# Kernel tuning notes

Measured on AMD Instinct MI355X. Metric: run time of the kernel, lower is better.

## Reference

```python
import jax, jax.numpy as jnp
import numpy as np

B, T, D = 2, 2048, 1024
N, K, H = 16, 8, 128  # q heads, kv heads, head_dim
G = N // K            # GQA group size
EPS = 1e-6
THETA = 1000000.0
SCALE = H ** -0.5
K_MASK = float(np.finfo(np.float32).min)


def rms_norm(x, scale):
    # RMSNorm over head_dim (last axis), computed in fp32 like the original
    dtype = x.dtype
    rms = jnp.sqrt(jnp.mean(x.astype(jnp.float32) ** 2, axis=-1, keepdims=True) + EPS)
    return (scale * x / rms).astype(dtype)


def positions_from_segment_ids(seg):
    t = jnp.arange(seg.shape[1], dtype=jnp.int32)[None, :]
    off = jnp.argmax(seg, axis=1, keepdims=True).astype(jnp.int32)
    rel = t - off
    return jnp.where(seg != 0, rel, jnp.int32(2 ** 30))


def rope_sin_cos(positions):
    frac = jnp.arange(0, H, 2, dtype=jnp.float32) / H
    inv_freq = 1.0 / (THETA ** frac)                    # [H/2]
    ang = positions.astype(jnp.float32)[..., None] * inv_freq  # [B,T,H/2]
    return jnp.sin(ang), jnp.cos(ang)


def apply_rope(x, sin, cos):
    # x: [B,T,heads,H]; sin/cos: [B,T,H/2]
    x1, x2 = x[..., : H // 2], x[..., H // 2:]
    s, c = sin[:, :, None, :], cos[:, :, None, :]
    return jnp.concatenate([x1 * c - x2 * s, x2 * c + x1 * s], axis=-1).astype(x.dtype)


def setup_inputs() -> dict:
    key = jax.random.key(0)
    ks = jax.random.split(key, 8)
    std = 0.02
    return {
        "x": jax.random.normal(ks[0], (B, T, D), dtype=jnp.float32),
        "segment_ids": jnp.ones((B, T), dtype=jnp.int32),
        "wq": jax.random.normal(ks[1], (D, N, H), dtype=jnp.float32) * std,
        "wk": jax.random.normal(ks[2], (D, K, H), dtype=jnp.float32) * std,
        "wv": jax.random.normal(ks[3], (D, K, H), dtype=jnp.float32) * std,
        "wo": jax.random.normal(ks[4], (N, H, D), dtype=jnp.float32) * std,
        "q_scale": jnp.ones((H,), dtype=jnp.float32),
        "k_scale": jnp.ones((H,), dtype=jnp.float32),
    }


def reference(x, segment_ids, wq, wk, wv, wo, q_scale, k_scale):
    # QKV projections + QK RMSNorm
    q = rms_norm(jnp.einsum('BTD,DNH->BTNH', x, wq), q_scale)  # [B,T,N,H]
    k = rms_norm(jnp.einsum('BSD,DKH->BSKH', x, wk), k_scale)  # [B,T,K,H]
    v = jnp.einsum('BSD,DKH->BSKH', x, wv)                     # [B,T,K,H]

    # RoPE using segment-relative positions
    pos = positions_from_segment_ids(segment_ids)  # [B,T] int32
    sin, cos = rope_sin_cos(pos)
    q = apply_rope(q, sin, cos)
    k = apply_rope(k, sin, cos)

    # GQA attention: [B,T,K,G,H] x [B,S,K,H] -> [B,T,S,K,G]
    qg = q.reshape(B, T, K, G, H)
    logits = jnp.einsum('BTKGH,BSKH->BTSKG', qg, k) * SCALE

    causal = pos[:, None, :] <= pos[:, :, None]                       # [B,T,S]
    segm = segment_ids[:, None, :] == segment_ids[:, :, None]         # [B,T,S]
    mask = (causal & segm)[:, :, :, None, None]
    logits = jnp.where(mask, logits, K_MASK)

    w = jax.nn.softmax(logits.astype(jnp.float32), axis=2).astype(logits.dtype)
    out = jnp.einsum('BTSKG,BSKH->BTKGH', w, v).reshape(B, T, N, H)
    return jnp.einsum('BTNH,NHD->BTD', out, wo)
```

## Files before the change

kernel.cpp:

```cpp
#include <hip/hip_runtime.h>
#include <hip/hip_bf16.h>


typedef unsigned short u16;
typedef __attribute__((ext_vector_type(8))) short s16x8;
typedef __attribute__((ext_vector_type(4))) float fp32x4;
typedef __attribute__((ext_vector_type(4))) u16 u16x4;

#define MFMA_BF16(a, b, c) __builtin_amdgcn_mfma_f32_16x16x32_bf16((a), (b), (c), 0, 0, 0)

static constexpr int Bq = 2, Tq = 2048, Dq = 1024, NHq = 16, KHq = 8, Hq = 128;
static constexpr float EPSq = 1e-6f;
static constexpr float S2q = 0.08838834764831845f * 1.4426950408889634f;
static constexpr float MAXq = 20.0f;
static constexpr float NEGHUGE = -3.0e38f;

__device__ __forceinline__ u16 f2b(float f) {
  __hip_bfloat16 h = __float2bfloat16(f);
  return *reinterpret_cast<u16*>(&h);
}

__device__ __forceinline__ void gload16(const u16* g, u16* lds_base) {
  __builtin_amdgcn_global_load_lds(
      (const __attribute__((address_space(1))) unsigned int*)(const void*)g,
      (__attribute__((address_space(3))) unsigned int*)(void*)lds_base, 16, 0, 0);
}


__global__ __launch_bounds__(256) void prep_kernel(
    const float* __restrict__ x, const float* __restrict__ wq,
    const float* __restrict__ wk, const float* __restrict__ wv,
    const float* __restrict__ wo, const int* __restrict__ seg,
    u16* __restrict__ xb, u16* __restrict__ wqkv_t, u16* __restrict__ wo_t,
    int* __restrict__ pos) {
  const int bid = blockIdx.x;
  const int tid = threadIdx.x;
  if (bid < 4096) {
    const int i = bid * 1024 + tid * 4;
    const float4 v = *reinterpret_cast<const float4*>(x + i);
    u16x4 o;
    o.x = f2b(v.x); o.y = f2b(v.y); o.z = f2b(v.z); o.w = f2b(v.w);
    *reinterpret_cast<u16x4*>(xb + i) = o;
    return;
  }
  __shared__ float tile[32][33];
  __shared__ int sv[256], si[256];
  const int tx = tid & 31, ty = tid >> 5;
  if (bid < 8192) {
    const int z = bid - 4096;
    const int r0 = (z & 31) * 32;
    const int c0 = (z >> 5) * 32;
    const float* src;
    int stride, coff;
    if (c0 < 2048)      { src = wq; stride = 2048; coff = c0; }
    else if (c0 < 3072) { src = wk; stride = 1024; coff = c0 - 2048; }
    else                { src = wv; stride = 1024; coff = c0 - 3072; }
#pragma unroll
    for (int j = 0; j < 32; j += 8)
      tile[ty + j][tx] = src[(long)(r0 + ty + j) * stride + (coff + tx)];
    __syncthreads();
#pragma unroll
    for (int j = 0; j < 32; j += 8)
      wqkv_t[(long)(c0 + ty + j) * 1024 + (r0 + tx)] = f2b(tile[tx][ty + j]);
    return;
  }
  if (bid < 10240) {
    const int z = bid - 8192;
    const int c0 = (z & 31) * 32;
    const int r0 = (z >> 5) * 32;
#pragma unroll
    for (int j = 0; j < 32; j += 8)
      tile[ty + j][tx] = wo[(long)(r0 + ty + j) * 1024 + (c0 + tx)];
    __syncthreads();
#pragma unroll
    for (int j = 0; j < 32; j += 8)
      wo_t[(long)(c0 + ty + j) * 2048 + (r0 + tx)] = f2b(tile[tx][ty + j]);
    return;
  }
  const int b = bid - 10240;
  const int* s = seg + b * Tq;
  int bestv = -2147483647 - 1, besti = 0x7fffffff;
  for (int t = tid; t < Tq; t += 256) {
    int v = s[t];
    if (v > bestv) { bestv = v; besti = t; }
  }
  sv[tid] = bestv; si[tid] = besti;
  __syncthreads();
  for (int k = 128; k > 0; k >>= 1) {
    if (tid < k) {
      int v2 = sv[tid + k], i2 = si[tid + k];
      if (v2 > sv[tid] || (v2 == sv[tid] && i2 < si[tid])) {
        sv[tid] = v2; si[tid] = i2;
      }
    }
    __syncthreads();
  }
  const int off = si[0];
  for (int t = tid; t < Tq; t += 256)
    pos[b * Tq + t] = (s[t] != 0) ? (t - off) : (1 << 30);
}


__global__ __launch_bounds__(256) void gemm_qkv_kernel(
    const u16* __restrict__ A, const u16* __restrict__ Bt,
    u16* __restrict__ qkv, u16* __restrict__ vt, const int* __restrict__ pos,
    const float* __restrict__ q_scale, const float* __restrict__ k_scale) {
  __shared__ __align__(16) u16 As[128][64];
  __shared__ __align__(16) u16 Bs[128][64];
  const int tid = threadIdx.x;
  const int wave = tid >> 6, lane = tid & 63;
  const int quad = lane >> 4, l16 = lane & 15;
  const int m0 = blockIdx.y * 128, n0 = blockIdx.x * 128;
  const int row8 = lane >> 3;
  const int cgl = (lane & 7) ^ row8;

  const fp32x4 z4 = {0.f, 0.f, 0.f, 0.f};
  fp32x4 acc[2][8];
#pragma unroll
  for (int i = 0; i < 2; ++i)
#pragma unroll
    for (int j = 0; j < 8; ++j) acc[i][j] = z4;

  for (int k0 = 0; k0 < 1024; k0 += 64) {
    __syncthreads();
#pragma unroll
    for (int jj = 0; jj < 4; ++jj) {
      const int R = wave * 32 + jj * 8;
      gload16(A + (size_t)(m0 + R + row8) * 1024 + k0 + cgl * 8, &As[R][0]);
      gload16(Bt + (size_t)(n0 + R + row8) * 1024 + k0 + cgl * 8, &Bs[R][0]);
    }
    __syncthreads();
#pragma unroll
    for (int kh = 0; kh < 2; ++kh) {
      s16x8 af[2], bfr[8];
#pragma unroll
      for (int i = 0; i < 2; ++i)
        af[i] = *(const s16x8*)&As[wave * 32 + i * 16 + l16]
                               [((((kh << 2) | quad) ^ (l16 & 7)) << 3)];
#pragma unroll
      for (int j = 0; j < 8; ++j)
        bfr[j] = *(const s16x8*)&Bs[j * 16 + l16]
                                [((((kh << 2) | quad) ^ (l16 & 7)) << 3)];
#pragma unroll
      for (int i = 0; i < 2; ++i)
#pragma unroll
        for (int j = 0; j < 8; ++j) acc[i][j] = MFMA_BF16(af[i], bfr[j], acc[i][j]);
    }
  }

  const int wrow = m0 + wave * 32;
  if (n0 >= 3072) {
    const int kv8 = (n0 - 3072) >> 7;
    const int bq = wrow >> 11;
    const size_t vbase = (size_t)(bq * KHq + kv8) * Hq * Tq;
#pragma unroll
    for (int i = 0; i < 2; ++i) {
      const int t = (wrow + i * 16 + quad * 4) & 2047;
#pragma unroll
      for (int j = 0; j < 8; ++j) {
        const int h = j * 16 + l16;
        u16x4 o;
#pragma unroll
        for (int r = 0; r < 4; ++r) o[r] = f2b(acc[i][j][r]);
        *reinterpret_cast<u16x4*>(&vt[vbase + (size_t)h * Tq + t]) = o;
      }
    }
    return;
  }
  const float* scp = (n0 < 2048) ? q_scale : k_scale;
  float scl[8];
#pragma unroll
  for (int j = 0; j < 8; ++j) scl[j] = scp[j * 16 + l16];
  float invf[4];
#pragma unroll
  for (int jf = 0; jf < 4; ++jf)
    invf[jf] = __builtin_amdgcn_exp2f(
                   -(float)(jf * 16 + l16) * (19.931568569324174f / 64.0f)) *
               0.15915494309189535f;
#pragma unroll
  for (int i = 0; i < 2; ++i) {
    float ss[4] = {0.f, 0.f, 0.f, 0.f};
#pragma unroll
    for (int j = 0; j < 8; ++j)
#pragma unroll
      for (int r = 0; r < 4; ++r) ss[r] += acc[i][j][r] * acc[i][j][r];
#pragma unroll
    for (int d = 1; d < 16; d <<= 1)
#pragma unroll
      for (int r = 0; r < 4; ++r) ss[r] += __shfl_xor(ss[r], d, 64);
#pragma unroll
    for (int r = 0; r < 4; ++r) {
      const int row = wrow + i * 16 + quad * 4 + r;
      const float rinv = rsqrtf(ss[r] * (1.0f / 128.0f) + EPSq);
      const float P = (float)pos[row];
      u16* orow = qkv + (size_t)row * 4096 + n0;
#pragma unroll
      for (int jf = 0; jf < 4; ++jf) {
        float rev = P * invf[jf];
        rev -= floorf(rev);
        const float s = __builtin_amdgcn_sinf(rev);
        const float c = __builtin_amdgcn_cosf(rev);
        const float a1 = acc[i][jf][r] * rinv * scl[jf];
        const float a2 = acc[i][jf + 4][r] * rinv * scl[jf + 4];
        orow[jf * 16 + l16] = f2b(a1 * c - a2 * s);
        orow[(jf + 4) * 16 + l16] = f2b(a2 * c + a1 * s);
      }
    }
  }
}


__global__ __launch_bounds__(256) void gemm_out_kernel(
    const u16* __restrict__ A, const u16* __restrict__ Bt,
    float* __restrict__ C) {
  __shared__ __align__(16) u16 As[128][64];
  __shared__ __align__(16) u16 Bs[64][64];
  const int tid = threadIdx.x;
  const int wave = tid >> 6, lane = tid & 63;
  const int quad = lane >> 4, l16 = lane & 15;
  const int m0 = blockIdx.y * 128, n0 = blockIdx.x * 64;
  const int wm = (wave >> 1) * 64, wn = (wave & 1) * 32;
  const int row8 = lane >> 3;
  const int cgl = (lane & 7) ^ row8;

  const fp32x4 z4 = {0.f, 0.f, 0.f, 0.f};
  fp32x4 acc[4][2];
#pragma unroll
  for (int i = 0; i < 4; ++i)
#pragma unroll
    for (int j = 0; j < 2; ++j) acc[i][j] = z4;

  for (int k0 = 0; k0 < 2048; k0 += 64) {
    __syncthreads();
#pragma unroll
    for (int jj = 0; jj < 4; ++jj) {
      const int R = wave * 32 + jj * 8;
      gload16(A + (size_t)(m0 + R + row8) * 2048 + k0 + cgl * 8, &As[R][0]);
    }
#pragma unroll
    for (int jj = 0; jj < 2; ++jj) {
      const int R = wave * 16 + jj * 8;
      gload16(Bt + (size_t)(n0 + R + row8) * 2048 + k0 + cgl * 8, &Bs[R][0]);
    }
    __syncthreads();
#pragma unroll
    for (int kh = 0; kh < 2; ++kh) {
      s16x8 af[4], bfr[2];
#pragma unroll
      for (int i = 0; i < 4; ++i)
        af[i] = *(const s16x8*)&As[wm + i * 16 + l16]
                               [((((kh << 2) | quad) ^ (l16 & 7)) << 3)];
#pragma unroll
      for (int j = 0; j < 2; ++j)
        bfr[j] = *(const s16x8*)&Bs[wn + j * 16 + l16]
                                [((((kh << 2) | quad) ^ (l16 & 7)) << 3)];
#pragma unroll
      for (int i = 0; i < 4; ++i)
#pragma unroll
        for (int j = 0; j < 2; ++j) acc[i][j] = MFMA_BF16(af[i], bfr[j], acc[i][j]);
    }
  }
#pragma unroll
  for (int i = 0; i < 4; ++i) {
    const int row = m0 + wm + i * 16 + quad * 4;
#pragma unroll
    for (int j = 0; j < 2; ++j) {
      const int col = n0 + wn + j * 16 + l16;
#pragma unroll
      for (int r = 0; r < 4; ++r)
        C[(size_t)(row + r) * 1024 + col] = acc[i][j][r];
    }
  }
}


__global__ __launch_bounds__(256, 1) void flash_kernel(
    const u16* __restrict__ qkv, const u16* __restrict__ vt,
    const int* __restrict__ pos, const int* __restrict__ seg,
    u16* __restrict__ Obuf) {
  const int tid = threadIdx.x;
  const int w = tid >> 6;
  const int lane = tid & 63;
  const int quad = lane >> 4, l16 = lane & 15;
  const int g = blockIdx.x;
  const int b = g & 1;
  const int kv = (g >> 1) & 7;
  const int qh = kv * 2 + ((g >> 4) & 1);
  const int p = g >> 5;

  __shared__ __align__(16) u16 Ks[2][64][128];
  __shared__ __align__(16) u16 Vs[2][128][64];
  __shared__ __align__(16) u16 Ps[4][32][72];

  const u16* kbase = qkv + (size_t)(b * Tq) * 4096 + 2048 + kv * Hq;
  const u16* vbase = vt + (size_t)(b * KHq + kv) * Hq * Tq;
  const int krow_off = lane >> 4;
  const int vrow_off = lane >> 3;
  const fp32x4 z4 = {0.f, 0.f, 0.f, 0.f};
  const short one_bf = (short)0x3F80;
  const s16x8 ones = {one_bf, one_bf, one_bf, one_bf,
                      one_bf, one_bf, one_bf, one_bf};

  auto STAGE = [&](int bi, int st) {
    const int s0 = st * 64;
#pragma unroll
    for (int j = 0; j < 4; ++j) {
      const int R = w * 16 + j * 4;
      const int r = R + krow_off;
      const int cg = (lane & 15) ^ (r & 15);
      gload16(kbase + (size_t)(s0 + r) * 4096 + cg * 8, &Ks[bi][R][0]);
    }
#pragma unroll
    for (int j = 0; j < 4; ++j) {
      const int R = w * 32 + j * 8;
      const int r = R + vrow_off;
      const int cg = (lane & 7) ^ (vrow_off & 7);
      gload16(vbase + (size_t)r * Tq + s0 + cg * 8, &Vs[bi][R][0]);
    }
  };

#pragma unroll
  for (int phase = 0; phase < 2; ++phase) {
    const int c = phase ? p : 15 - p;
    const int t0 = c * 128 + w * 32;
    const int nst = 2 * (c + 1);

    s16x8 qf[2][4];
    int my_pos[2][4], my_seg[2][4];
#pragma unroll
    for (int rb = 0; rb < 2; ++rb) {
      const u16* qrow =
          qkv + (size_t)(b * Tq + t0 + rb * 16 + l16) * 4096 + qh * Hq;
#pragma unroll
      for (int ks = 0; ks < 4; ++ks)
        qf[rb][ks] = *(const s16x8*)(qrow + ks * 32 + quad * 8);
#pragma unroll
      for (int i = 0; i < 4; ++i) {
        const int t = t0 + rb * 16 + quad * 4 + i;
        my_pos[rb][i] = pos[b * Tq + t];
        my_seg[rb][i] = seg[b * Tq + t];
      }
    }
    fp32x4 l_acc[2] = {z4, z4};
    fp32x4 o_acc[2][8];
#pragma unroll
    for (int rb = 0; rb < 2; ++rb)
#pragma unroll
      for (int h = 0; h < 8; ++h) o_acc[rb][h] = z4;

    STAGE(0, 0);
    __syncthreads();

    for (int st = 0; st < nst; ++st) {
      const int cur = st & 1;
      if (st + 1 < nst) STAGE(cur ^ 1, st + 1);

      fp32x4 sc[2][4];
#pragma unroll
      for (int rb = 0; rb < 2; ++rb)
#pragma unroll
        for (int sub = 0; sub < 4; ++sub) sc[rb][sub] = z4;
#pragma unroll
      for (int sub = 0; sub < 4; ++sub)
#pragma unroll
        for (int ks = 0; ks < 4; ++ks) {
          const s16x8 kf = *(const s16x8*)&Ks[cur][sub * 16 + l16]
                                             [((((ks << 2) | quad) ^ l16) << 3)];
          sc[0][sub] = MFMA_BF16(qf[0][ks], kf, sc[0][sub]);
          sc[1][sub] = MFMA_BF16(qf[1][ks], kf, sc[1][sub]);
        }

      const int s0 = st * 64;
      if (st >= nst - 2) {
        int spos[4], sseg[4];
#pragma unroll
        for (int sub = 0; sub < 4; ++sub) {
          const int s = s0 + sub * 16 + l16;
          spos[sub] = pos[b * Tq + s];
          sseg[sub] = seg[b * Tq + s];
        }
#pragma unroll
        for (int rb = 0; rb < 2; ++rb)
#pragma unroll
          for (int sub = 0; sub < 4; ++sub)
#pragma unroll
            for (int i = 0; i < 4; ++i) {
              const bool ok = (sseg[sub] == my_seg[rb][i]) &&
                              (spos[sub] <= my_pos[rb][i]);
              sc[rb][sub][i] = ok ? sc[rb][sub][i] * S2q - MAXq : NEGHUGE;
            }
      } else {
#pragma unroll
        for (int rb = 0; rb < 2; ++rb)
#pragma unroll
          for (int sub = 0; sub < 4; ++sub)
#pragma unroll
            for (int i = 0; i < 4; ++i)
              sc[rb][sub][i] = sc[rb][sub][i] * S2q - MAXq;
      }

#pragma unroll
      for (int rb = 0; rb < 2; ++rb)
#pragma unroll
        for (int sub = 0; sub < 4; ++sub)
#pragma unroll
          for (int i = 0; i < 4; ++i)
            Ps[w][rb * 16 + quad * 4 + i][sub * 16 + l16] =
                f2b(__builtin_amdgcn_exp2f(sc[rb][sub][i]));
      asm volatile("s_waitcnt lgkmcnt(0)" ::: "memory");
      s16x8 pf[2][2];
#pragma unroll
      for (int rb = 0; rb < 2; ++rb)
#pragma unroll
        for (int kk = 0; kk < 2; ++kk)
          pf[rb][kk] = *(const s16x8*)&Ps[w][rb * 16 + l16][kk * 32 + quad * 8];

      l_acc[0] = MFMA_BF16(pf[0][0], ones, l_acc[0]);
      l_acc[0] = MFMA_BF16(pf[0][1], ones, l_acc[0]);
      l_acc[1] = MFMA_BF16(pf[1][0], ones, l_acc[1]);
      l_acc[1] = MFMA_BF16(pf[1][1], ones, l_acc[1]);
#pragma unroll
      for (int j = 0; j < 8; ++j)
#pragma unroll
        for (int kk = 0; kk < 2; ++kk) {
          const s16x8 vf =
              *(const s16x8*)&Vs[cur][j * 16 + l16]
                             [((((kk << 2) | quad) ^ (l16 & 7)) << 3)];
          o_acc[0][j] = MFMA_BF16(pf[0][kk], vf, o_acc[0][j]);
          o_acc[1][j] = MFMA_BF16(pf[1][kk], vf, o_acc[1][j]);
        }

      __syncthreads();
    }

#pragma unroll
    for (int rb = 0; rb < 2; ++rb) {
      float inv[4];
#pragma unroll
      for (int i = 0; i < 4; ++i)
        inv[i] = (l_acc[rb][i] > 0.f) ? 1.f / l_acc[rb][i] : 0.f;
#pragma unroll
      for (int j = 0; j < 8; ++j)
#pragma unroll
        for (int i = 0; i < 4; ++i) {
          const int t = t0 + rb * 16 + quad * 4 + i;
          Obuf[(size_t)(b * Tq + t) * 2048 + qh * Hq + j * 16 + l16] =
              f2b(o_acc[rb][j][i] * inv[i]);
        }
    }
  }
}


extern "C" void kernel_launch(void* const* d_in, const int* in_sizes, int n_in,
                              void* d_out, int out_size, void* d_ws, size_t ws_size,
                              hipStream_t stream) {
  const float* x = (const float*)d_in[0];
  const int* seg = (const int*)d_in[1];
  const float* wq = (const float*)d_in[2];
  const float* wk = (const float*)d_in[3];
  const float* wv = (const float*)d_in[4];
  const float* wo = (const float*)d_in[5];
  const float* q_scale = (const float*)d_in[6];
  const float* k_scale = (const float*)d_in[7];
  float* out = (float*)d_out;

  char* ws = (char*)d_ws;
  u16* xb = (u16*)(ws);
  u16* wqkv_t = (u16*)(ws + 8388608);
  u16* qkv = (u16*)(ws + 16777216);
  u16* vt = (u16*)(ws + 50331648);
  u16* wo_t = (u16*)(ws + 58720256);
  u16* Obuf = (u16*)(ws + 62914560);
  int* posb = (int*)(ws + 79691776);

  prep_kernel<<<10242, 256, 0, stream>>>(x, wq, wk, wv, wo, seg,
                                         xb, wqkv_t, wo_t, posb);

  gemm_qkv_kernel<<<dim3(32, 32, 1), 256, 0, stream>>>(
      xb, wqkv_t, qkv, vt, posb, q_scale, k_scale);

  flash_kernel<<<256, 256, 0, stream>>>(qkv, vt, posb, seg, Obuf);

  gemm_out_kernel<<<dim3(16, 32, 1), 256, 0, stream>>>(Obuf, wo_t, out);
}
```

Before: 235.0 us.

## Split flash kernel causal phases into separate blocks and drop LDS double buffering

Each flash block previously handled two query chunks (c and 15-p) sequentially with double-buffered K/V LDS staging. Now the grid doubles to 512 blocks, each handling one chunk, K/V staging becomes single-buffered with syncs around each load, and launch bounds allow two blocks per CU. The aim is more resident waves and latency hiding through occupancy instead of in-block prefetch. The cost is that loads are no longer overlapped with compute inside a block, and per-block work is now unbalanced across the causal chunks.

After: 237.9 us. Within noise of the previous version (+1.2%).

```diff
diff --git a/kernel.cpp b/kernel.cpp
--- a/kernel.cpp
+++ b/kernel.cpp
@@ -274,7 +274,7 @@
 }
 
 
-__global__ __launch_bounds__(256, 1) void flash_kernel(
+__global__ __launch_bounds__(256, 2) void flash_kernel(
     const u16* __restrict__ qkv, const u16* __restrict__ vt,
     const int* __restrict__ pos, const int* __restrict__ seg,
     u16* __restrict__ Obuf) {
@@ -283,13 +283,17 @@
   const int lane = tid & 63;
   const int quad = lane >> 4, l16 = lane & 15;
   const int g = blockIdx.x;
-  const int b = g & 1;
-  const int kv = (g >> 1) & 7;
-  const int qh = kv * 2 + ((g >> 4) & 1);
-  const int p = g >> 5;
-
-  __shared__ __align__(16) u16 Ks[2][64][128];
-  __shared__ __align__(16) u16 Vs[2][128][64];
+  const int u = g & 255;
+  const int b = u & 1;
+  const int kv = (u >> 1) & 7;
+  const int qh = kv * 2 + ((u >> 4) & 1);
+  const int p = u >> 5;
+  const int c = (g >> 8) ? p : 15 - p;
+  const int t0 = c * 128 + w * 32;
+  const int nst = 2 * (c + 1);
+
+  __shared__ __align__(16) u16 Ks[64][128];
+  __shared__ __align__(16) u16 Vs[128][64];
   __shared__ __align__(16) u16 Ps[4][32][72];
 
   const u16* kbase = qkv + (size_t)(b * Tq) * 4096 + 2048 + kv * Hq;
@@ -301,153 +305,137 @@
   const s16x8 ones = {one_bf, one_bf, one_bf, one_bf,
                       one_bf, one_bf, one_bf, one_bf};
 
-  auto STAGE = [&](int bi, int st) {
+  s16x8 qf[2][4];
+  int my_pos[2][4], my_seg[2][4];
+#pragma unroll
+  for (int rb = 0; rb < 2; ++rb) {
+    const u16* qrow =
+        qkv + (size_t)(b * Tq + t0 + rb * 16 + l16) * 4096 + qh * Hq;
+#pragma unroll
+    for (int ks = 0; ks < 4; ++ks)
+      qf[rb][ks] = *(const s16x8*)(qrow + ks * 32 + quad * 8);
+#pragma unroll
+    for (int i = 0; i < 4; ++i) {
+      const int t = t0 + rb * 16 + quad * 4 + i;
+      my_pos[rb][i] = pos[b * Tq + t];
+      my_seg[rb][i] = seg[b * Tq + t];
+    }
+  }
+  fp32x4 l_acc[2] = {z4, z4};
+  fp32x4 o_acc[2][8];
+#pragma unroll
+  for (int rb = 0; rb < 2; ++rb)
+#pragma unroll
+    for (int h = 0; h < 8; ++h) o_acc[rb][h] = z4;
+
+  for (int st = 0; st < nst; ++st) {
     const int s0 = st * 64;
+    __syncthreads();
 #pragma unroll
     for (int j = 0; j < 4; ++j) {
       const int R = w * 16 + j * 4;
       const int r = R + krow_off;
       const int cg = (lane & 15) ^ (r & 15);
-      gload16(kbase + (size_t)(s0 + r) * 4096 + cg * 8, &Ks[bi][R][0]);
+      gload16(kbase + (size_t)(s0 + r) * 4096 + cg * 8, &Ks[R][0]);
     }
 #pragma unroll
     for (int j = 0; j < 4; ++j) {
       const int R = w * 32 + j * 8;
       const int r = R + vrow_off;
       const int cg = (lane & 7) ^ (vrow_off & 7);
-      gload16(vbase + (size_t)r * Tq + s0 + cg * 8, &Vs[bi][R][0]);
-    }
-  };
-
-#pragma unroll
-  for (int phase = 0; phase < 2; ++phase) {
-    const int c = phase ? p : 15 - p;
-    const int t0 = c * 128 + w * 32;
-    const int nst = 2 * (c + 1);
-
-    s16x8 qf[2][4];
-    int my_pos[2][4], my_seg[2][4];
-#pragma unroll
-    for (int rb = 0; rb < 2; ++rb) {
-      const u16* qrow =
-          qkv + (size_t)(b * Tq + t0 + rb * 16 + l16) * 4096 + qh * Hq;
-#pragma unroll
-      for (int ks = 0; ks < 4; ++ks)
-        qf[rb][ks] = *(const s16x8*)(qrow + ks * 32 + quad * 8);
+      gload16(vbase + (size_t)r * Tq + s0 + cg * 8, &Vs[R][0]);
+    }
+    __syncthreads();
+
+    fp32x4 sc[2][4];
+#pragma unroll
+    for (int rb = 0; rb < 2; ++rb)
+#pragma unroll
+      for (int sub = 0; sub < 4; ++sub) sc[rb][sub] = z4;
+#pragma unroll
+    for (int sub = 0; sub < 4; ++sub)
+#pragma unroll
+      for (int ks = 0; ks < 4; ++ks) {
+        const s16x8 kf = *(const s16x8*)&Ks[sub * 16 + l16]
+                                           [((((ks << 2) | quad) ^ l16) << 3)];
+        sc[0][sub] = MFMA_BF16(qf[0][ks], kf, sc[0][sub]);
+        sc[1][sub] = MFMA_BF16(qf[1][ks], kf, sc[1][sub]);
+      }
+
+    if (st >= nst - 2) {
+      int spos[4], sseg[4];
+#pragma unroll
+      for (int sub = 0; sub < 4; ++sub) {
+        const int s = s0 + sub * 16 + l16;
+        spos[sub] = pos[b * Tq + s];
+        sseg[sub] = seg[b * Tq + s];
+      }
+#pragma unroll
+      for (int rb = 0; rb < 2; ++rb)
+#pragma unroll
+        for (int sub = 0; sub < 4; ++sub)
+#pragma unroll
+          for (int i = 0; i < 4; ++i) {
+            const bool ok = (sseg[sub] == my_seg[rb][i]) &&
+                            (spos[sub] <= my_pos[rb][i]);
+            sc[rb][sub][i] = ok ? sc[rb][sub][i] * S2q - MAXq : NEGHUGE;
+          }
+    } else {
+#pragma unroll
+      for (int rb = 0; rb < 2; ++rb)
+#pragma unroll
+        for (int sub = 0; sub < 4; ++sub)
+#pragma unroll
+          for (int i = 0; i < 4; ++i)
+            sc[rb][sub][i] = sc[rb][sub][i] * S2q - MAXq;
+    }
+
+#pragma unroll
+    for (int rb = 0; rb < 2; ++rb)
+#pragma unroll
+      for (int sub = 0; sub < 4; ++sub)
+#pragma unroll
+        for (int i = 0; i < 4; ++i)
+          Ps[w][rb * 16 + quad * 4 + i][sub * 16 + l16] =
+              f2b(__builtin_amdgcn_exp2f(sc[rb][sub][i]));
+    asm volatile("s_waitcnt lgkmcnt(0)" ::: "memory");
+    s16x8 pf[2][2];
+#pragma unroll
+    for (int rb = 0; rb < 2; ++rb)
+#pragma unroll
+      for (int kk = 0; kk < 2; ++kk)
+        pf[rb][kk] = *(const s16x8*)&Ps[w][rb * 16 + l16][kk * 32 + quad * 8];
+
+    l_acc[0] = MFMA_BF16(pf[0][0], ones, l_acc[0]);
+    l_acc[0] = MFMA_BF16(pf[0][1], ones, l_acc[0]);
+    l_acc[1] = MFMA_BF16(pf[1][0], ones, l_acc[1]);
+    l_acc[1] = MFMA_BF16(pf[1][1], ones, l_acc[1]);
+#pragma unroll
+    for (int j = 0; j < 8; ++j)
+#pragma unroll
+      for (int kk = 0; kk < 2; ++kk) {
+        const s16x8 vf =
+            *(const s16x8*)&Vs[j * 16 + l16]
+                           [((((kk << 2) | quad) ^ (l16 & 7)) << 3)];
+        o_acc[0][j] = MFMA_BF16(pf[0][kk], vf, o_acc[0][j]);
+        o_acc[1][j] = MFMA_BF16(pf[1][kk], vf, o_acc[1][j]);
+      }
+  }
+
+#pragma unroll
+  for (int rb = 0; rb < 2; ++rb) {
+    float inv[4];
+#pragma unroll
+    for (int i = 0; i < 4; ++i)
+      inv[i] = (l_acc[rb][i] > 0.f) ? 1.f / l_acc[rb][i] : 0.f;
+#pragma unroll
+    for (int j = 0; j < 8; ++j)
 #pragma unroll
       for (int i = 0; i < 4; ++i) {
         const int t = t0 + rb * 16 + quad * 4 + i;
-        my_pos[rb][i] = pos[b * Tq + t];
-        my_seg[rb][i] = seg[b * Tq + t];
-      }
-    }
-    fp32x4 l_acc[2] = {z4, z4};
-    fp32x4 o_acc[2][8];
-#pragma unroll
-    for (int rb = 0; rb < 2; ++rb)
-#pragma unroll
-      for (int h = 0; h < 8; ++h) o_acc[rb][h] = z4;
-
-    STAGE(0, 0);
-    __syncthreads();
-
-    for (int st = 0; st < nst; ++st) {
-      const int cur = st & 1;
-      if (st + 1 < nst) STAGE(cur ^ 1, st + 1);
-
-      fp32x4 sc[2][4];
-#pragma unroll
-      for (int rb = 0; rb < 2; ++rb)
-#pragma unroll
-        for (int sub = 0; sub < 4; ++sub) sc[rb][sub] = z4;
-#pragma unroll
-      for (int sub = 0; sub < 4; ++sub)
-#pragma unroll
-        for (int ks = 0; ks < 4; ++ks) {
-          const s16x8 kf = *(const s16x8*)&Ks[cur][sub * 16 + l16]
-                                             [((((ks << 2) | quad) ^ l16) << 3)];
-          sc[0][sub] = MFMA_BF16(qf[0][ks], kf, sc[0][sub]);
-          sc[1][sub] = MFMA_BF16(qf[1][ks], kf, sc[1][sub]);
-        }
-
-      const int s0 = st * 64;
-      if (st >= nst - 2) {
-        int spos[4], sseg[4];
-#pragma unroll
-        for (int sub = 0; sub < 4; ++sub) {
-          const int s = s0 + sub * 16 + l16;
-          spos[sub] = pos[b * Tq + s];
-          sseg[sub] = seg[b * Tq + s];
-        }
-#pragma unroll
-        for (int rb = 0; rb < 2; ++rb)
-#pragma unroll
-          for (int sub = 0; sub < 4; ++sub)
-#pragma unroll
-            for (int i = 0; i < 4; ++i) {
-              const bool ok = (sseg[sub] == my_seg[rb][i]) &&
-                              (spos[sub] <= my_pos[rb][i]);
-              sc[rb][sub][i] = ok ? sc[rb][sub][i] * S2q - MAXq : NEGHUGE;
-            }
-      } else {
-#pragma unroll
-        for (int rb = 0; rb < 2; ++rb)
-#pragma unroll
-          for (int sub = 0; sub < 4; ++sub)
-#pragma unroll
-            for (int i = 0; i < 4; ++i)
-              sc[rb][sub][i] = sc[rb][sub][i] * S2q - MAXq;
-      }
-
-#pragma unroll
-      for (int rb = 0; rb < 2; ++rb)
-#pragma unroll
-        for (int sub = 0; sub < 4; ++sub)
-#pragma unroll
-          for (int i = 0; i < 4; ++i)
-            Ps[w][rb * 16 + quad * 4 + i][sub * 16 + l16] =
-                f2b(__builtin_amdgcn_exp2f(sc[rb][sub][i]));
-      asm volatile("s_waitcnt lgkmcnt(0)" ::: "memory");
-      s16x8 pf[2][2];
-#pragma unroll
-      for (int rb = 0; rb < 2; ++rb)
-#pragma unroll
-        for (int kk = 0; kk < 2; ++kk)
-          pf[rb][kk] = *(const s16x8*)&Ps[w][rb * 16 + l16][kk * 32 + quad * 8];
-
-      l_acc[0] = MFMA_BF16(pf[0][0], ones, l_acc[0]);
-      l_acc[0] = MFMA_BF16(pf[0][1], ones, l_acc[0]);
-      l_acc[1] = MFMA_BF16(pf[1][0], ones, l_acc[1]);
-      l_acc[1] = MFMA_BF16(pf[1][1], ones, l_acc[1]);
-#pragma unroll
-      for (int j = 0; j < 8; ++j)
-#pragma unroll
-        for (int kk = 0; kk < 2; ++kk) {
-          const s16x8 vf =
-              *(const s16x8*)&Vs[cur][j * 16 + l16]
-                             [((((kk << 2) | quad) ^ (l16 & 7)) << 3)];
-          o_acc[0][j] = MFMA_BF16(pf[0][kk], vf, o_acc[0][j]);
-          o_acc[1][j] = MFMA_BF16(pf[1][kk], vf, o_acc[1][j]);
-        }
-
-      __syncthreads();
-    }
-
-#pragma unroll
-    for (int rb = 0; rb < 2; ++rb) {
-      float inv[4];
-#pragma unroll
-      for (int i = 0; i < 4; ++i)
-        inv[i] = (l_acc[rb][i] > 0.f) ? 1.f / l_acc[rb][i] : 0.f;
-#pragma unroll
-      for (int j = 0; j < 8; ++j)
-#pragma unroll
-        for (int i = 0; i < 4; ++i) {
-          const int t = t0 + rb * 16 + quad * 4 + i;
-          Obuf[(size_t)(b * Tq + t) * 2048 + qh * Hq + j * 16 + l16] =
-              f2b(o_acc[rb][j][i] * inv[i]);
-        }
-    }
+        Obuf[(size_t)(b * Tq + t) * 2048 + qh * Hq + j * 16 + l16] =
+            f2b(o_acc[rb][j][i] * inv[i]);
+      }
   }
 }
 
@@ -480,7 +468,7 @@
   gemm_qkv_kernel<<<dim3(32, 32, 1), 256, 0, stream>>>(
       xb, wqkv_t, qkv, vt, posb, q_scale, k_scale);
 
-  flash_kernel<<<256, 256, 0, stream>>>(qkv, vt, posb, seg, Obuf);
+  flash_kernel<<<512, 256, 0, stream>>>(qkv, vt, posb, seg, Obuf);
 
   gemm_out_kernel<<<dim3(16, 32, 1), 256, 0, stream>>>(Obuf, wo_t, out);
 }
```
